# Optimization experiments

Hardware: AMD Instinct MI355X
Metric: run time of the kernel (lower is better)

## Reference

```python
import jax, jax.numpy as jnp
import numpy as np

H = 256  # rnn_size


def setup_inputs() -> dict:
    key = jax.random.key(0)
    ks = jax.random.split(key, 6)
    B, T, F, D = 64, 512, 64, 64
    s_in = 1.0 / np.sqrt(F)
    s_rec = 1.0 / np.sqrt(H)
    return {
        "x": jax.random.normal(ks[0], (B, T, F), jnp.float32),
        "kernel": jax.random.normal(ks[1], (F, 3 * H), jnp.float32) * s_in,
        "recurrent_kernel": jax.random.normal(ks[2], (H, 3 * H), jnp.float32) * s_rec,
        "bias": jax.random.normal(ks[3], (3 * H,), jnp.float32) * 0.01,
        "dense_w": jax.random.normal(ks[4], (H, D), jnp.float32) * s_rec,
        "dense_b": jax.random.normal(ks[5], (D,), jnp.float32) * 0.01,
    }


def _gru_scan(x, kernel, recurrent_kernel, bias):
    B, T, _ = x.shape
    # Pre-project all timesteps: [B, T, 3H]
    xproj = jnp.einsum("btf,fg->btg", x, kernel) + bias
    xproj_t = jnp.transpose(xproj, (1, 0, 2))  # [T, B, 3H]

    def step(h, xt):
        # Keras GRU, reset_after=False: r gates the recurrent matmul of the candidate
        rec = h @ recurrent_kernel  # [B, 3H]
        xz, xr, xh = xt[:, :H], xt[:, H:2 * H], xt[:, 2 * H:]
        rz, rr, rh = rec[:, :H], rec[:, H:2 * H], rec[:, 2 * H:]
        z = jax.nn.sigmoid(xz + rz)
        r = jax.nn.sigmoid(xr + rr)
        hh = jnp.tanh(xh + r * rh)
        h_new = z * h + (1.0 - z) * hh
        return h_new, h_new

    h0 = jnp.zeros((B, H), x.dtype)
    h_last, outs = jax.lax.scan(step, h0, xproj_t)
    return jnp.transpose(outs, (1, 0, 2)), h_last  # [B,T,H], [B,H]


def reference(x, kernel, recurrent_kernel, bias, dense_w, dense_b):
    outputs, h_last = _gru_scan(x, kernel, recurrent_kernel, bias)
    state = jnp.tanh(h_last @ dense_w + dense_b)  # [B, dense_size]
    return outputs, state
```

## Files before the change

### kernel.cpp

```cpp
#include <hip/hip_runtime.h>


typedef _Float16 half2_t __attribute__((ext_vector_type(2)));
typedef _Float16 f16x4_t __attribute__((ext_vector_type(4)));

#define LOG2E 1.4426950408889634f

__device__ __forceinline__ float fast_sigmoid(float x) {
  float e = __builtin_amdgcn_exp2f(-x * LOG2E);
  return __builtin_amdgcn_rcpf(1.0f + e);
}
__device__ __forceinline__ float fast_tanh(float x) {
  float e = __builtin_amdgcn_exp2f(x * (2.0f * LOG2E));
  return 1.0f - 2.0f * __builtin_amdgcn_rcpf(1.0f + e);
}

__global__ __launch_bounds__(256, 4) void xproj_gemm(
    const float* __restrict__ x, const float* __restrict__ kmat,
    const float* __restrict__ bias, _Float16* __restrict__ xp) {
  __shared__ half2_t As2[32][132];
  __shared__ half2_t Bs2[32][132];
  const int tid = threadIdx.x;
  const int rb = blockIdx.x * 128;
  const int cb = blockIdx.y * 128;

  {
    const int k4 = (tid & 15) * 4;
    const int r0 = tid >> 4;
#pragma unroll
    for (int p = 0; p < 8; ++p) {
      int r = r0 + p * 16;
      float4 v = *(const float4*)(x + (size_t)(rb + r) * 64 + k4);
      half2_t lo, hi;
      lo[0] = (_Float16)v.x; lo[1] = (_Float16)v.y;
      hi[0] = (_Float16)v.z; hi[1] = (_Float16)v.w;
      As2[k4 / 2][r] = lo;
      As2[k4 / 2 + 1][r] = hi;
    }
  }
  {
    const int c4 = (tid & 31) * 4;
    const int kp0 = tid >> 5;
#pragma unroll
    for (int p = 0; p < 4; ++p) {
      int kp = kp0 + p * 8;
      float4 va = *(const float4*)(kmat + (size_t)(2 * kp) * 768 + cb + c4);
      float4 vb = *(const float4*)(kmat + (size_t)(2 * kp + 1) * 768 + cb + c4);
      half2_t o0, o1, o2, o3;
      o0[0] = (_Float16)va.x; o0[1] = (_Float16)vb.x;
      o1[0] = (_Float16)va.y; o1[1] = (_Float16)vb.y;
      o2[0] = (_Float16)va.z; o2[1] = (_Float16)vb.z;
      o3[0] = (_Float16)va.w; o3[1] = (_Float16)vb.w;
      Bs2[kp][c4 + 0] = o0;
      Bs2[kp][c4 + 1] = o1;
      Bs2[kp][c4 + 2] = o2;
      Bs2[kp][c4 + 3] = o3;
    }
  }
  __syncthreads();

  const int tx = tid & 15, ty = tid >> 4;
  const int r0 = ty * 8;
  const int c0 = tx * 4;
  float acc[8][8];
  {
    float4 b0 = *(const float4*)(bias + cb + c0);
    float4 b1 = *(const float4*)(bias + cb + 64 + c0);
    float bz[8] = {b0.x, b0.y, b0.z, b0.w, b1.x, b1.y, b1.z, b1.w};
#pragma unroll
    for (int i = 0; i < 8; ++i)
#pragma unroll
      for (int j = 0; j < 8; ++j) acc[i][j] = bz[j];
  }

#pragma unroll 2
  for (int kp = 0; kp < 32; ++kp) {
    half2_t a2[8], b2[8];
    *(int4*)(&a2[0]) = *(const int4*)(&As2[kp][r0]);
    *(int4*)(&a2[4]) = *(const int4*)(&As2[kp][r0 + 4]);
    *(int2*)(&b2[0]) = *(const int2*)(&Bs2[kp][c0]);
    *(int2*)(&b2[2]) = *(const int2*)(&Bs2[kp][c0 + 2]);
    *(int2*)(&b2[4]) = *(const int2*)(&Bs2[kp][64 + c0]);
    *(int2*)(&b2[6]) = *(const int2*)(&Bs2[kp][64 + c0 + 2]);
#pragma unroll
    for (int i = 0; i < 8; ++i)
#pragma unroll
      for (int j = 0; j < 8; ++j)
        acc[i][j] = __builtin_amdgcn_fdot2(a2[i], b2[j], acc[i][j], false);
  }

#pragma unroll
  for (int i = 0; i < 8; ++i) {
    f16x4_t o0, o1;
#pragma unroll
    for (int j = 0; j < 4; ++j) {
      o0[j] = (_Float16)acc[i][j];
      o1[j] = (_Float16)acc[i][4 + j];
    }
    _Float16* dst = xp + (size_t)(rb + r0 + i) * 768 + cb;
    *(f16x4_t*)(dst + c0) = o0;
    *(f16x4_t*)(dst + 64 + c0) = o1;
  }
}

__global__ __launch_bounds__(1024, 4) void gru_scan(
    const _Float16* __restrict__ xp, const float* __restrict__ wr,
    const float* __restrict__ dw, const float* __restrict__ db,
    float* __restrict__ out, float* __restrict__ state) {
  __shared__ float part[4 * 768];
  __shared__ float hbuf[256];
  __shared__ alignas(16) _Float16 hhalf[256];
  __shared__ _Float16 xrow[768];

  const int tid = threadIdx.x;
  const int b = blockIdx.x;
  const int c = tid >> 8;
  const int col = tid & 255;

  half2_t w2[3][32];
#pragma unroll
  for (int q = 0; q < 3; ++q) {
    const float* wp = wr + (size_t)(c * 64) * 768 + col + q * 256;
#pragma unroll
    for (int j = 0; j < 32; ++j) {
      float wa = wp[(size_t)(2 * j) * 768];
      float wb = wp[(size_t)(2 * j + 1) * 768];
      half2_t p;
      p[0] = (_Float16)wa;
      p[1] = (_Float16)wb;
      w2[q][j] = p;
    }
  }

  if (tid < 256) hhalf[tid] = (_Float16)0.0f;
  __syncthreads();

  const _Float16* xpb = xp + (size_t)b * 512 * 768;
  float* outb = out + (size_t)b * 512 * 256;
  const int4* hp2 = (const int4*)hhalf + c * 8;
  float hprev = 0.0f;

  for (int t = 0; t < 512; ++t) {
    _Float16 xv = (_Float16)0.0f;
    if (tid < 768) xv = xpb[(size_t)t * 768 + tid];

    float a0 = 0.0f, a1 = 0.0f, a2 = 0.0f;
    int4 hv = hp2[0];
#pragma unroll
    for (int g = 0; g < 8; ++g) {
      __builtin_amdgcn_sched_barrier(1);
      int4 hn = hv;
      if (g < 7) hn = hp2[g + 1];
      half2_t p0 = __builtin_bit_cast(half2_t, hv.x);
      half2_t p1 = __builtin_bit_cast(half2_t, hv.y);
      half2_t p2 = __builtin_bit_cast(half2_t, hv.z);
      half2_t p3 = __builtin_bit_cast(half2_t, hv.w);
      a0 = __builtin_amdgcn_fdot2(p0, w2[0][g * 4 + 0], a0, false);
      a0 = __builtin_amdgcn_fdot2(p1, w2[0][g * 4 + 1], a0, false);
      a0 = __builtin_amdgcn_fdot2(p2, w2[0][g * 4 + 2], a0, false);
      a0 = __builtin_amdgcn_fdot2(p3, w2[0][g * 4 + 3], a0, false);
      a1 = __builtin_amdgcn_fdot2(p0, w2[1][g * 4 + 0], a1, false);
      a1 = __builtin_amdgcn_fdot2(p1, w2[1][g * 4 + 1], a1, false);
      a1 = __builtin_amdgcn_fdot2(p2, w2[1][g * 4 + 2], a1, false);
      a1 = __builtin_amdgcn_fdot2(p3, w2[1][g * 4 + 3], a1, false);
      a2 = __builtin_amdgcn_fdot2(p0, w2[2][g * 4 + 0], a2, false);
      a2 = __builtin_amdgcn_fdot2(p1, w2[2][g * 4 + 1], a2, false);
      a2 = __builtin_amdgcn_fdot2(p2, w2[2][g * 4 + 2], a2, false);
      a2 = __builtin_amdgcn_fdot2(p3, w2[2][g * 4 + 3], a2, false);
      hv = hn;
    }
    part[c * 768 + col] = a0;
    part[c * 768 + col + 256] = a1;
    part[c * 768 + col + 512] = a2;
    if (tid < 768) xrow[tid] = xv;
    __syncthreads();

    if (tid < 256) {
      const int i = tid;
      if (t) outb[(size_t)(t - 1) * 256 + i] = hprev;
      float rz = part[i] + part[768 + i] + part[1536 + i] + part[2304 + i];
      float rr = part[256 + i] + part[768 + 256 + i] + part[1536 + 256 + i] +
                 part[2304 + 256 + i];
      float rh = part[512 + i] + part[768 + 512 + i] + part[1536 + 512 + i] +
                 part[2304 + 512 + i];
      float xz = (float)xrow[i];
      float xr = (float)xrow[256 + i];
      float xh = (float)xrow[512 + i];
      float z = fast_sigmoid(xz + rz);
      float r = fast_sigmoid(xr + rr);
      float hh = fast_tanh(xh + r * rh);
      float hnew = z * hprev + (1.0f - z) * hh;
      hprev = hnew;
      hhalf[i] = (_Float16)hnew;
    }
    __syncthreads();
  }

  if (tid < 256) {
    outb[(size_t)511 * 256 + tid] = hprev;
    hbuf[tid] = hprev;
  }
  __syncthreads();

  if (tid < 64) {
    float acc = db[tid];
#pragma unroll 8
    for (int k = 0; k < 256; ++k) acc = fmaf(hbuf[k], dw[k * 64 + tid], acc);
    state[(size_t)b * 64 + tid] = fast_tanh(acc);
  }
}

extern "C" void kernel_launch(void* const* d_in, const int* in_sizes, int n_in,
                              void* d_out, int out_size, void* d_ws,
                              size_t ws_size, hipStream_t stream) {
  const float* x = (const float*)d_in[0];
  const float* kmat = (const float*)d_in[1];
  const float* wr = (const float*)d_in[2];
  const float* bias = (const float*)d_in[3];
  const float* dw = (const float*)d_in[4];
  const float* db = (const float*)d_in[5];

  float* out = (float*)d_out;
  float* state = out + (size_t)64 * 512 * 256;
  _Float16* xp = (_Float16*)d_ws;

  dim3 gg(32768 / 128, 768 / 128);
  xproj_gemm<<<gg, 256, 0, stream>>>(x, kmat, bias, xp);
  gru_scan<<<64, 1024, 0, stream>>>(xp, wr, dw, db, out, state);
}
```

Baseline: 661.9 us.

## Split GRU recurrent matvec across two K-halves instead of four

The scan block shrinks from 1024 to 512 threads, so each thread holds twice as many recurrent weight pairs in registers (192 half2) and covers a 128-long K slice. The reduction becomes a single shared-memory partial plus the thread's own accumulator, and the x-projection values are loaded directly into registers by the gate threads instead of staged through shared memory. This cuts shared-memory traffic, reduction adds and the number of waves taking part in each barrier. In exchange the serial dot-product chain per step doubles in length and register pressure rises, which risks spills.

```diff
diff --git a/kernel.cpp b/kernel.cpp
--- a/kernel.cpp
+++ b/kernel.cpp
@@ -103,26 +103,25 @@
   }
 }
 
-__global__ __launch_bounds__(1024, 4) void gru_scan(
+__global__ __launch_bounds__(512, 2) void gru_scan(
     const _Float16* __restrict__ xp, const float* __restrict__ wr,
     const float* __restrict__ dw, const float* __restrict__ db,
     float* __restrict__ out, float* __restrict__ state) {
-  __shared__ float part[4 * 768];
+  __shared__ float part[3 * 256];
   __shared__ float hbuf[256];
   __shared__ alignas(16) _Float16 hhalf[256];
-  __shared__ _Float16 xrow[768];
 
   const int tid = threadIdx.x;
   const int b = blockIdx.x;
   const int c = tid >> 8;
   const int col = tid & 255;
 
-  half2_t w2[3][32];
+  half2_t w2[3][64];
 #pragma unroll
   for (int q = 0; q < 3; ++q) {
-    const float* wp = wr + (size_t)(c * 64) * 768 + col + q * 256;
-#pragma unroll
-    for (int j = 0; j < 32; ++j) {
+    const float* wp = wr + (size_t)(c * 128) * 768 + col + q * 256;
+#pragma unroll
+    for (int j = 0; j < 64; ++j) {
       float wa = wp[(size_t)(2 * j) * 768];
       float wb = wp[(size_t)(2 * j + 1) * 768];
       half2_t p;
@@ -137,20 +136,24 @@
 
   const _Float16* xpb = xp + (size_t)b * 512 * 768;
   float* outb = out + (size_t)b * 512 * 256;
-  const int4* hp2 = (const int4*)hhalf + c * 8;
+  const int4* hp = (const int4*)hhalf + c * 16;
   float hprev = 0.0f;
 
   for (int t = 0; t < 512; ++t) {
-    _Float16 xv = (_Float16)0.0f;
-    if (tid < 768) xv = xpb[(size_t)t * 768 + tid];
+    float xz = 0.0f, xr = 0.0f, xh = 0.0f;
+    if (tid < 256) {
+      const _Float16* xr0 = xpb + (size_t)t * 768 + tid;
+      xz = (float)xr0[0];
+      xr = (float)xr0[256];
+      xh = (float)xr0[512];
+    }
 
     float a0 = 0.0f, a1 = 0.0f, a2 = 0.0f;
-    int4 hv = hp2[0];
-#pragma unroll
-    for (int g = 0; g < 8; ++g) {
-      __builtin_amdgcn_sched_barrier(1);
+    int4 hv = hp[0];
+#pragma unroll
+    for (int g = 0; g < 16; ++g) {
       int4 hn = hv;
-      if (g < 7) hn = hp2[g + 1];
+      if (g < 15) hn = hp[g + 1];
       half2_t p0 = __builtin_bit_cast(half2_t, hv.x);
       half2_t p1 = __builtin_bit_cast(half2_t, hv.y);
       half2_t p2 = __builtin_bit_cast(half2_t, hv.z);
@@ -169,23 +172,19 @@
       a2 = __builtin_amdgcn_fdot2(p3, w2[2][g * 4 + 3], a2, false);
       hv = hn;
     }
-    part[c * 768 + col] = a0;
-    part[c * 768 + col + 256] = a1;
-    part[c * 768 + col + 512] = a2;
-    if (tid < 768) xrow[tid] = xv;
+    if (tid >= 256) {
+      part[col] = a0;
+      part[256 + col] = a1;
+      part[512 + col] = a2;
+    }
     __syncthreads();
 
     if (tid < 256) {
       const int i = tid;
       if (t) outb[(size_t)(t - 1) * 256 + i] = hprev;
-      float rz = part[i] + part[768 + i] + part[1536 + i] + part[2304 + i];
-      float rr = part[256 + i] + part[768 + 256 + i] + part[1536 + 256 + i] +
-                 part[2304 + 256 + i];
-      float rh = part[512 + i] + part[768 + 512 + i] + part[1536 + 512 + i] +
-                 part[2304 + 512 + i];
-      float xz = (float)xrow[i];
-      float xr = (float)xrow[256 + i];
-      float xh = (float)xrow[512 + i];
+      float rz = a0 + part[i];
+      float rr = a1 + part[256 + i];
+      float rh = a2 + part[512 + i];
       float z = fast_sigmoid(xz + rz);
       float r = fast_sigmoid(xr + rr);
       float hh = fast_tanh(xh + r * rh);
@@ -226,5 +225,5 @@
 
   dim3 gg(32768 / 128, 768 / 128);
   xproj_gemm<<<gg, 256, 0, stream>>>(x, kmat, bias, xp);
-  gru_scan<<<64, 1024, 0, stream>>>(xp, wr, dw, db, out, state);
-}
+  gru_scan<<<64, 512, 0, stream>>>(xp, wr, dw, db, out, state);
+}
```

New measurement: 707.5 us. 1.07x slower.
